# Kernel optimization log

Hardware: AMD Instinct MI355X
Metric: run time of the kernel (lower is better)

The kernel has to match this reference:

```python
import jax, jax.numpy as jnp
import numpy as np
from jax import lax

# ---- module hyperparams (from __init__ defaults) ----
REF_TR = 2.0
NUM_BANDS = 5
FREQ_LO, FREQ_HI = 0.008, 0.12

# ---- pywt.cwt('morl') internals, precision=10 ----
NPSI = 1024                                   # 2**10 samples of the wavelet
_x = np.linspace(-8.0, 8.0, NPSI)             # morlet support [-8, 8]
STEP = float(_x[1] - _x[0])
DOMAIN = 16.0                                 # x[-1] - x[0]
_psi = np.exp(-_x ** 2 / 2.0) * np.cos(5.0 * _x)   # 'morl' wavelet psi(t)
INT_PSI = jnp.asarray(np.cumsum(_psi) * STEP, dtype=jnp.float32)  # integrate_wavelet
LMAX = 544                                    # static bound: max scale ~33.4 -> L <= 535


def _cwt_band(gpad, scale):
    """pywt conv-method CWT at one scale for all regions.
    gpad: [R, N+1+2*LMAX] = first difference of zero-extended signal, zero-padded.
    Uses identity: diff(convolve(x, K[::-1])) == correlate(diff-ext(x), K) shifted.
    """
    R = gpad.shape[0]
    N = gpad.shape[1] - 1 - 2 * LMAX
    i = jnp.arange(LMAX)
    # len(np.arange(scale*16 + 1)) for non-integer scale*16
    L0 = jnp.floor(scale * DOMAIN).astype(jnp.int32) + 2
    j = jnp.floor(i.astype(jnp.float32) / (scale * STEP)).astype(jnp.int32)
    mask = (i < L0) & (j < NPSI)              # pywt filters j < int_psi.size
    K = jnp.where(mask, INT_PSI[jnp.clip(j, 0, NPSI - 1)], 0.0)  # int_psi_scale (unreversed)
    L = mask.sum()                            # effective kernel length (mask is a prefix)
    # cross-correlation of gpad with K (lax.conv does correlation, no kernel flip)
    corr = lax.conv_general_dilated(gpad[:, None, :], K[None, None, :], (1,), 'VALID',
                                    dimension_numbers=('NCH', 'OIH', 'NCH'))[:, 0, :]
    # center crop: coef[t] = -sqrt(s) * (c[t+f+1]-c[t+f]),  f = floor((L-2)/2)
    start = LMAX + (L - 2) // 2 + 2 - L
    coef = lax.dynamic_slice(corr, (jnp.int32(0), start), (R, N))
    return jnp.abs(-jnp.sqrt(scale) * coef)


def _forward(timeseries, tr_values, log_scale_params, bandwidth_params):
    B, R, N = timeseries.shape
    tr_factors = tr_values / REF_TR
    scales = jnp.exp(log_scale_params)[None, :] / tr_factors[:, None]      # [B, bands]
    # frequency bands [B, bands, 2]
    center = 1.0 / (scales * tr_values[:, None])
    bw = bandwidth_params[None, :]
    low = jnp.maximum(FREQ_LO, center * (1.0 - bw / 2.0))
    high = jnp.minimum(FREQ_HI, center * (1.0 + bw / 2.0))
    frequency_bands = jnp.stack([low, high], axis=-1)
    # first difference of zero-extended signal: g[m] = x[m] - x[m-1], x=0 outside [0,N)
    g = jnp.diff(jnp.pad(timeseries, ((0, 0), (0, 0), (1, 1))), axis=-1)    # [B,R,N+1]
    gpad = jnp.pad(g, ((0, 0), (0, 0), (LMAX, LMAX)))
    per_sample = jax.vmap(_cwt_band, in_axes=(None, 0))                     # over bands
    coeffs = jax.vmap(per_sample, in_axes=(0, 0))(gpad, scales)             # [B,bands,R,N]
    coeffs = jnp.transpose(coeffs, (0, 2, 1, 3))                            # [B,R,bands,N]
    return coeffs, frequency_bands


def setup_inputs() -> dict:
    key = jax.random.key(0)
    k1, k2 = jax.random.split(key)
    B, R, T = 8, 400, 1200
    timeseries = jax.random.normal(k1, (B, R, T), dtype=jnp.float32)
    # realistic fMRI TRs in [1.5, 2.5] s (keeps adaptive scales <= 33.4 < LMAX/16)
    tr_values = 1.5 + jax.random.uniform(k2, (B,), dtype=jnp.float32)
    log_scale_params = jnp.linspace(np.log(5.0), np.log(25.0), NUM_BANDS).astype(jnp.float32)
    bandwidth_params = 0.1 * jnp.ones((NUM_BANDS,), dtype=jnp.float32)
    return {"timeseries": timeseries, "tr_values": tr_values,
            "log_scale_params": log_scale_params, "bandwidth_params": bandwidth_params}


def reference(timeseries, tr_values, log_scale_params, bandwidth_params):
    return _forward(timeseries, tr_values, log_scale_params, bandwidth_params)
```

## Files before the change

### kernel.cpp

```cpp
#include <hip/hip_runtime.h>
#include <math.h>

#define B_    8
#define R_    400
#define N_    1200
#define S_    5
#define LMAX_ 544
#define NPSI_ 1024
#define KPAD  560
#define WINMAX 1760
#define T_    20

#define WS_K      1024
#define WS_SCALE  (WS_K + 40*KPAD)
#define WS_SQS    (WS_SCALE + 40)
#define WS_L      (WS_SQS + 40)
#define WS_START  (WS_L + 40)

__global__ void setup_kernel(const float* __restrict__ tr,
                             const float* __restrict__ lsp,
                             const float* __restrict__ bwp,
                             float* __restrict__ ws,
                             float* __restrict__ out_bands)
{
    __shared__ double psi_sh[NPSI_];
    const double STEP_D = 16.0 / 1023.0;
    const float  STEP_F = (float)(16.0 / 1023.0);
    const int tid = threadIdx.x;

    for (int k = tid; k < NPSI_; k += 256) {
        double x = (k == NPSI_ - 1) ? 8.0 : (-8.0 + (double)k * STEP_D);
        psi_sh[k] = exp(-x * x * 0.5) * cos(5.0 * x);
    }
    __syncthreads();

    if (tid == 0) {
        double c = 0.0;
        for (int k = 0; k < NPSI_; ++k) {
            c += psi_sh[k];
            ws[k] = (float)(c * STEP_D);
        }
    }
    __syncthreads();

    float* scale_arr = ws + WS_SCALE;
    float* sqs_arr   = ws + WS_SQS;
    int*   L_arr     = (int*)(ws + WS_L);
    int*   start_arr = (int*)(ws + WS_START);

    if (tid < 40) {
        int b = tid / S_, s = tid % S_;
        float trf   = tr[b] / 2.0f;
        float scale = expf(lsp[s]) / trf;
        float sst   = scale * STEP_F;
        int   L0    = (int)floorf(scale * 16.0f) + 2;
        int   L     = 0;
        for (int i = 0; i < LMAX_; ++i) {
            int j = (int)floorf((float)i / sst);
            if (i < L0 && j < NPSI_) ++L;
        }
        scale_arr[tid] = scale;
        sqs_arr[tid]   = sqrtf(scale);
        L_arr[tid]     = L;
        start_arr[tid] = LMAX_ + (L - 2) / 2 + 2 - L;

        float center = 1.0f / (scale * tr[b]);
        float bw     = bwp[s];
        float lo = fmaxf(0.008f, center * (1.0f - bw / 2.0f));
        float hi = fminf(0.12f,  center * (1.0f + bw / 2.0f));
        out_bands[tid * 2 + 0] = lo;
        out_bands[tid * 2 + 1] = hi;
    }
    __syncthreads();

    for (int idx = tid; idx < 40 * KPAD; idx += 256) {
        int p = idx / KPAD;
        int i = idx % KPAD;
        float v = 0.0f;
        if (i < LMAX_) {
            float scale = scale_arr[p];
            float sst   = scale * STEP_F;
            int   L0    = (int)floorf(scale * 16.0f) + 2;
            int   j     = (int)floorf((float)i / sst);
            if (i < L0 && j < NPSI_) {
                int jc = j < 0 ? 0 : (j > NPSI_ - 1 ? NPSI_ - 1 : j);
                v = ws[jc];
            }
        }
        ws[WS_K + idx] = v;
    }
}

__global__ __launch_bounds__(256) void cwt_main_kernel(
    const float* __restrict__ ts,
    const float* __restrict__ ws,
    float* __restrict__ out)
{
    const float* Kbase     = ws + WS_K;
    const float* sqs_arr   = ws + WS_SQS;
    const int*   L_arr     = (const int*)(ws + WS_L);
    const int*   start_arr = (const int*)(ws + WS_START);

    const int bid = blockIdx.x;
    const int rg  = bid % 100;
    const int b   = (bid / 100) % B_;
    const int s   = 4 - (bid / (100 * B_));
    const int pair = b * S_ + s;

    const int   L      = L_arr[pair];
    const int   start  = start_arr[pair];
    const float sqs    = sqs_arr[pair];
    const int   wstart = start - LMAX_;
    const int   Lpad   = ((L + T_ - 1) / T_) * T_;

    __shared__ __align__(16) float gwin[4][WINMAX];

    const int tid = threadIdx.x;

    for (int wv = 0; wv < 4; ++wv) {
        const int r = rg * 4 + wv;
        const float* tsrow = ts + (size_t)(b * R_ + r) * N_;
        for (int t = tid; t < WINMAX; t += 256) {
            int k = wstart + t;
            float v = 0.0f;
            if (k >= 0 && k <= N_) {
                float a = (k < N_) ? tsrow[k]     : 0.0f;
                float c = (k > 0)  ? tsrow[k - 1] : 0.0f;
                v = a - c;
            }
            gwin[wv][t] = v;
        }
    }
    __syncthreads();

    const int wv = tid >> 6;
    const int ln = tid & 63;
    const int t0 = T_ * (ln < 60 ? ln : 59);
    const float* gw = gwin[wv];
    const float* Kp = Kbase + pair * KPAD;

    float acc[T_];
    #pragma unroll
    for (int q = 0; q < T_; ++q) acc[q] = 0.0f;

    for (int i = 0; i < Lpad; i += T_) {
        float kk[T_];
        #pragma unroll
        for (int m = 0; m < T_ / 4; ++m)
            *(float4*)&kk[4 * m] = *(const float4*)(Kp + i + 4 * m);

        float w[2 * T_];
        #pragma unroll
        for (int m = 0; m < 2 * T_ / 4; ++m)
            *(float4*)&w[4 * m] = *(const float4*)(gw + t0 + i + 4 * m);

        #pragma unroll
        for (int q = 0; q < T_; ++q) {
            #pragma unroll
            for (int j = 0; j < T_; ++j)
                acc[q] = fmaf(kk[j], w[q + j], acc[q]);
        }
    }

    if (ln < 60) {
        const int r = rg * 4 + wv;
        float* op = out + ((size_t)(b * R_ + r) * S_ + s) * N_ + t0;
        #pragma unroll
        for (int m = 0; m < T_ / 4; ++m) {
            float4 v;
            v.x = sqs * fabsf(acc[4 * m + 0]);
            v.y = sqs * fabsf(acc[4 * m + 1]);
            v.z = sqs * fabsf(acc[4 * m + 2]);
            v.w = sqs * fabsf(acc[4 * m + 3]);
            *(float4*)(op + 4 * m) = v;
        }
    }
}

extern "C" void kernel_launch(void* const* d_in, const int* in_sizes, int n_in,
                              void* d_out, int out_size, void* d_ws, size_t ws_size,
                              hipStream_t stream)
{
    const float* ts  = (const float*)d_in[0];
    const float* tr  = (const float*)d_in[1];
    const float* lsp = (const float*)d_in[2];
    const float* bwp = (const float*)d_in[3];
    float* out = (float*)d_out;
    float* ws  = (float*)d_ws;
    float* out_bands = out + (size_t)B_ * R_ * S_ * N_;

    hipLaunchKernelGGL(setup_kernel, dim3(1), dim3(256), 0, stream,
                       tr, lsp, bwp, ws, out_bands);
    hipLaunchKernelGGL(cwt_main_kernel, dim3(100 * B_ * S_), dim3(256), 0, stream,
                       ts, ws, out);
}
```

Baseline: 261.7 us.

## Parallelize setup scan and count, swizzle LDS window and use rolling register window

In the setup kernel, the single-thread cumulative sum is replaced by a wave-shuffle parallel prefix scan. The per-pair serial loop that computes kernel length is replaced by wave ballots with popcount and shared-memory atomics, which removes serial latency from the single-block setup launch. In the main convolution kernel, the shared-memory signal window gets an XOR swizzle on float4 groups to reduce bank conflicts. The inner loop now keeps a rolling 24-float register window, so each 24-tap step needs fewer LDS loads. The trade-off is kernel padding to multiples of 24, which adds a few wasted taps, plus more complex indexing.

```diff
diff --git a/kernel.cpp b/kernel.cpp
--- a/kernel.cpp
+++ b/kernel.cpp
@@ -11,80 +11,113 @@
 #define WINMAX 1760
 #define T_    20
 
-#define WS_K      1024
-#define WS_SCALE  (WS_K + 40*KPAD)
+#define WS_K      0
+#define WS_SCALE  (40*KPAD)
 #define WS_SQS    (WS_SCALE + 40)
 #define WS_L      (WS_SQS + 40)
 #define WS_START  (WS_L + 40)
 
-__global__ void setup_kernel(const float* __restrict__ tr,
-                             const float* __restrict__ lsp,
-                             const float* __restrict__ bwp,
-                             float* __restrict__ ws,
-                             float* __restrict__ out_bands)
+__device__ __forceinline__ float4 lds_ld4(const float* base, int dw) {
+    int g = dw >> 2;
+    g ^= (g >> 3) & 7;
+    return *(const float4*)(base + (g << 2));
+}
+
+__global__ __launch_bounds__(256) void setup_kernel(
+    const float* __restrict__ tr,
+    const float* __restrict__ lsp,
+    const float* __restrict__ bwp,
+    float* __restrict__ ws,
+    float* __restrict__ out_bands)
 {
     __shared__ double psi_sh[NPSI_];
+    __shared__ float  intpsi[NPSI_];
+    __shared__ double wtot[4];
+    __shared__ float  scale_sh[40];
+    __shared__ int    cnt_sh[40];
     const double STEP_D = 16.0 / 1023.0;
     const float  STEP_F = (float)(16.0 / 1023.0);
     const int tid = threadIdx.x;
 
+    if (tid < 40) cnt_sh[tid] = 0;
+
     for (int k = tid; k < NPSI_; k += 256) {
         double x = (k == NPSI_ - 1) ? 8.0 : (-8.0 + (double)k * STEP_D);
         psi_sh[k] = exp(-x * x * 0.5) * cos(5.0 * x);
     }
     __syncthreads();
 
-    if (tid == 0) {
-        double c = 0.0;
-        for (int k = 0; k < NPSI_; ++k) {
-            c += psi_sh[k];
-            ws[k] = (float)(c * STEP_D);
-        }
-    }
-    __syncthreads();
-
-    float* scale_arr = ws + WS_SCALE;
-    float* sqs_arr   = ws + WS_SQS;
-    int*   L_arr     = (int*)(ws + WS_L);
-    int*   start_arr = (int*)(ws + WS_START);
+    {
+        double a0 = psi_sh[4 * tid + 0], a1 = psi_sh[4 * tid + 1];
+        double a2 = psi_sh[4 * tid + 2], a3 = psi_sh[4 * tid + 3];
+        double s1 = a0 + a1, s2 = s1 + a2, s3 = s2 + a3;
+        double run = s3;
+        #pragma unroll
+        for (int d = 1; d < 64; d <<= 1) {
+            double o = __shfl_up(run, (unsigned)d, 64);
+            if ((tid & 63) >= d) run += o;
+        }
+        if ((tid & 63) == 63) wtot[tid >> 6] = run;
+        __syncthreads();
+        double woff = 0.0;
+        const int w = tid >> 6;
+        #pragma unroll
+        for (int k = 0; k < 4; ++k) if (k < w) woff += wtot[k];
+        double excl = woff + run - s3;
+        intpsi[4 * tid + 0] = (float)((excl + a0) * STEP_D);
+        intpsi[4 * tid + 1] = (float)((excl + s1) * STEP_D);
+        intpsi[4 * tid + 2] = (float)((excl + s2) * STEP_D);
+        intpsi[4 * tid + 3] = (float)((excl + s3) * STEP_D);
+    }
 
     if (tid < 40) {
         int b = tid / S_, s = tid % S_;
         float trf   = tr[b] / 2.0f;
         float scale = expf(lsp[s]) / trf;
-        float sst   = scale * STEP_F;
-        int   L0    = (int)floorf(scale * 16.0f) + 2;
-        int   L     = 0;
-        for (int i = 0; i < LMAX_; ++i) {
-            int j = (int)floorf((float)i / sst);
-            if (i < L0 && j < NPSI_) ++L;
-        }
-        scale_arr[tid] = scale;
-        sqs_arr[tid]   = sqrtf(scale);
-        L_arr[tid]     = L;
-        start_arr[tid] = LMAX_ + (L - 2) / 2 + 2 - L;
-
+        scale_sh[tid] = scale;
+        ws[WS_SCALE + tid] = scale;
+        ws[WS_SQS + tid]   = sqrtf(scale);
         float center = 1.0f / (scale * tr[b]);
-        float bw     = bwp[s];
-        float lo = fmaxf(0.008f, center * (1.0f - bw / 2.0f));
-        float hi = fminf(0.12f,  center * (1.0f + bw / 2.0f));
-        out_bands[tid * 2 + 0] = lo;
-        out_bands[tid * 2 + 1] = hi;
-    }
-    __syncthreads();
+        float bw = bwp[s];
+        out_bands[2 * tid + 0] = fmaxf(0.008f, center * (1.0f - bw * 0.5f));
+        out_bands[2 * tid + 1] = fminf(0.12f,  center * (1.0f + bw * 0.5f));
+    }
+    __syncthreads();
+
+    {
+        const int wv = tid >> 6, ln = tid & 63;
+        for (int c = wv; c < 40 * 9; c += 4) {
+            int p = c / 9, i = (c % 9) * 64 + ln;
+            float scale = scale_sh[p];
+            float sst   = scale * STEP_F;
+            int   L0    = (int)floorf(scale * 16.0f) + 2;
+            bool m = false;
+            if (i < LMAX_) {
+                int j = (int)floorf((float)i / sst);
+                m = (i < L0) && (j < NPSI_);
+            }
+            unsigned long long bal = __ballot(m);
+            if (ln == 0) atomicAdd(&cnt_sh[p], __popcll(bal));
+        }
+    }
+    __syncthreads();
+    if (tid < 40) {
+        int L = cnt_sh[tid];
+        ((int*)(ws + WS_L))[tid]     = L;
+        ((int*)(ws + WS_START))[tid] = LMAX_ + (L - 2) / 2 + 2 - L;
+    }
 
     for (int idx = tid; idx < 40 * KPAD; idx += 256) {
-        int p = idx / KPAD;
-        int i = idx % KPAD;
+        int p = idx / KPAD, i = idx % KPAD;
         float v = 0.0f;
         if (i < LMAX_) {
-            float scale = scale_arr[p];
+            float scale = scale_sh[p];
             float sst   = scale * STEP_F;
             int   L0    = (int)floorf(scale * 16.0f) + 2;
             int   j     = (int)floorf((float)i / sst);
             if (i < L0 && j < NPSI_) {
                 int jc = j < 0 ? 0 : (j > NPSI_ - 1 ? NPSI_ - 1 : j);
-                v = ws[jc];
+                v = intpsi[jc];
             }
         }
         ws[WS_K + idx] = v;
@@ -111,9 +144,9 @@
     const int   start  = start_arr[pair];
     const float sqs    = sqs_arr[pair];
     const int   wstart = start - LMAX_;
-    const int   Lpad   = ((L + T_ - 1) / T_) * T_;
-
-    __shared__ __align__(16) float gwin[4][WINMAX];
+    const int   Lpad   = ((L + 23) / 24) * 24;
+
+    __shared__ __align__(16) float gwin[4 * WINMAX];
 
     const int tid = threadIdx.x;
 
@@ -128,7 +161,10 @@
                 float c = (k > 0)  ? tsrow[k - 1] : 0.0f;
                 v = a - c;
             }
-            gwin[wv][t] = v;
+            int dw = wv * WINMAX + t;
+            int g  = dw >> 2;
+            g ^= (g >> 3) & 7;
+            gwin[(g << 2) | (dw & 3)] = v;
         }
     }
     __syncthreads();
@@ -136,29 +172,31 @@
     const int wv = tid >> 6;
     const int ln = tid & 63;
     const int t0 = T_ * (ln < 60 ? ln : 59);
-    const float* gw = gwin[wv];
+    const int dwbase = wv * WINMAX + t0;
     const float* Kp = Kbase + pair * KPAD;
 
     float acc[T_];
     #pragma unroll
     for (int q = 0; q < T_; ++q) acc[q] = 0.0f;
 
-    for (int i = 0; i < Lpad; i += T_) {
-        float kk[T_];
-        #pragma unroll
-        for (int m = 0; m < T_ / 4; ++m)
-            *(float4*)&kk[4 * m] = *(const float4*)(Kp + i + 4 * m);
-
-        float w[2 * T_];
-        #pragma unroll
-        for (int m = 0; m < 2 * T_ / 4; ++m)
-            *(float4*)&w[4 * m] = *(const float4*)(gw + t0 + i + 4 * m);
-
-        #pragma unroll
-        for (int q = 0; q < T_; ++q) {
+    float W[24];
+    #pragma unroll
+    for (int m = 0; m < 5; ++m)
+        *(float4*)&W[4 * m] = lds_ld4(gwin, dwbase + 4 * m);
+
+    for (int i = 0; i < Lpad; i += 24) {
+        #pragma unroll
+        for (int p = 0; p < 6; ++p) {
+            const int slot = (4 * p + 20) % 24;
+            *(float4*)&W[slot] = lds_ld4(gwin, dwbase + i + 4 * p + 20);
+            float4 k4 = *(const float4*)(Kp + i + 4 * p);
             #pragma unroll
-            for (int j = 0; j < T_; ++j)
-                acc[q] = fmaf(kk[j], w[q + j], acc[q]);
+            for (int j = 0; j < 4; ++j) {
+                const float kv = (j == 0) ? k4.x : (j == 1) ? k4.y : (j == 2) ? k4.z : k4.w;
+                #pragma unroll
+                for (int q = 0; q < T_; ++q)
+                    acc[q] = fmaf(kv, W[(4 * p + j + q) % 24], acc[q]);
+            }
         }
     }
 
```

Measured after the change: 238.7 us. 8.8% less time.
